# Performance work log

Measured on AMD Instinct MI355X. Metric: run time of the kernel, lower is better.

Reference implementation:

```python
import jax, jax.numpy as jnp
import numpy as np

B, S, IN, OUT, GS = 4, 2048, 4096, 4096, 256
NG = IN // GS  # number of groups per output channel


def setup_inputs() -> dict:
    key = jax.random.key(0)
    k1, k2, k3, k4 = jax.random.split(key, 4)
    x = jax.random.normal(k1, (B, S, IN), dtype=jnp.float32)
    # int4 codes stored in int8: values in [-8, 7]
    weight_int8 = jax.random.randint(k2, (OUT, IN), -8, 8, dtype=jnp.int32).astype(jnp.int8)
    scales = jax.random.uniform(k3, (OUT, NG), dtype=jnp.float32, minval=0.001, maxval=0.02)
    # zero points stored in scales_precision (float), integer-valued in int4 range
    zeros = jax.random.randint(k4, (OUT, NG), -8, 8, dtype=jnp.int32).astype(jnp.float32)
    return {"x": x, "weight_int8": weight_int8, "scales": scales, "zeros": zeros,
            "group_size": GS}


def per_token_dynamic_quant(x):
    """Asymmetric per-token int8 quantize -> dequantize (torchao decomposed ops)."""
    qmin, qmax = -128.0, 127.0
    mn = jnp.minimum(jnp.min(x, axis=-1, keepdims=True), 0.0)
    mx = jnp.maximum(jnp.max(x, axis=-1, keepdims=True), 0.0)
    eps = jnp.finfo(jnp.float32).eps
    scale = jnp.maximum((mx - mn) / (qmax - qmin), eps)
    # choose zero point minimizing error at whichever end is larger
    zp = jnp.where((qmin + mn / scale) + (qmax + mx / scale) > 0,
                   qmin - mn / scale, qmax - mx / scale)
    zp = jnp.clip(jnp.round(zp), qmin, qmax)
    q = jnp.clip(jnp.round(x / scale) + zp, qmin, qmax)
    return (q - zp) * scale


def dequant_per_channel_group(w_int8, scales, zeros, group_size):
    O, I = w_int8.shape
    g = I // group_size
    w = w_int8.reshape(O, g, group_size).astype(jnp.float32)
    w_dq = (w - zeros[:, :, None]) * scales[:, :, None]
    return w_dq.reshape(O, I)


def reference(x, weight_int8, scales, zeros, group_size):
    xq = per_token_dynamic_quant(x.astype(jnp.float32))
    w_dq = dequant_per_channel_group(weight_int8, scales, zeros, group_size)
    # F.linear: x @ w_dq.T  -> [B, S, OUT]
    return jnp.einsum('bsi,oi->bso', xq, w_dq)
```

## Files before the change

kernel.cpp:

```cpp
#include <hip/hip_runtime.h>
#include <hip/hip_bf16.h>
#include <stdint.h>

#define T_   8192
#define IN_  4096
#define OUT_ 4096
#define GS_  256
#define NG_  16

#define BM 128
#define BN 128
#define BK 64
#define KT (IN_ / BK)

typedef int   v4i __attribute__((ext_vector_type(4)));
typedef float f4  __attribute__((ext_vector_type(4)));

__device__ __forceinline__ void gload16(const void* g, void* l) {
  __builtin_amdgcn_global_load_lds(
      (const __attribute__((address_space(1))) void*)g,
      (__attribute__((address_space(3))) void*)l, 16, 0, 0);
}

__global__ __launch_bounds__(256) void quant_kernel(
    const float* __restrict__ x, int8_t* __restrict__ q,
    float* __restrict__ tscale, float* __restrict__ tzp) {
  const int t = blockIdx.x;
  const int tid = threadIdx.x;
  const float* xr = x + (size_t)t * IN_ + tid * 16;
  float vals[16];
  {
    f4 v0 = *(const f4*)(xr);
    f4 v1 = *(const f4*)(xr + 4);
    f4 v2 = *(const f4*)(xr + 8);
    f4 v3 = *(const f4*)(xr + 12);
#pragma unroll
    for (int i = 0; i < 4; ++i) {
      vals[i] = v0[i]; vals[4 + i] = v1[i]; vals[8 + i] = v2[i]; vals[12 + i] = v3[i];
    }
  }
  float mn = 0.f, mx = 0.f;
#pragma unroll
  for (int i = 0; i < 16; ++i) { mn = fminf(mn, vals[i]); mx = fmaxf(mx, vals[i]); }
#pragma unroll
  for (int off = 32; off > 0; off >>= 1) {
    mn = fminf(mn, __shfl_xor(mn, off));
    mx = fmaxf(mx, __shfl_xor(mx, off));
  }
  __shared__ float smn[4], smx[4];
  if ((tid & 63) == 0) { smn[tid >> 6] = mn; smx[tid >> 6] = mx; }
  __syncthreads();
  mn = fminf(fminf(smn[0], smn[1]), fminf(smn[2], smn[3]));
  mx = fmaxf(fmaxf(smx[0], smx[1]), fmaxf(smx[2], smx[3]));

  const float eps = 1.1920928955078125e-7f;
  float scale = fmaxf((mx - mn) / 255.0f, eps);
  float rmn = mn / scale;
  float rmx = mx / scale;
  float zp0 = ((-128.0f + rmn) + (127.0f + rmx) > 0.0f) ? (-128.0f - rmn)
                                                        : (127.0f - rmx);
  float zp = fminf(fmaxf(rintf(zp0), -128.0f), 127.0f);
  if (tid == 0) { tscale[t] = scale; tzp[t] = zp; }

  v4i packed;
#pragma unroll
  for (int w = 0; w < 4; ++w) {
    int word = 0;
#pragma unroll
    for (int e = 0; e < 4; ++e) {
      float qf = rintf(vals[w * 4 + e] / scale) + zp;
      qf = fminf(fmaxf(qf, -128.0f), 127.0f);
      int qi = (int)qf;
      word |= (qi & 0xff) << (8 * e);
    }
    packed[w] = word;
  }
  *(v4i*)(q + (size_t)t * IN_ + tid * 16) = packed;
}

__global__ __launch_bounds__(256) void wprep_kernel(
    const int* __restrict__ w, const float* __restrict__ scales,
    const float* __restrict__ zeros, int8_t* __restrict__ wq,
    float* __restrict__ c1) {
  const int o = blockIdx.x;
  const int tid = threadIdx.x;
  const int g = tid >> 4;
  const int* wr = w + (size_t)o * IN_ + tid * 16;
  const int zi = (int)zeros[o * NG_ + g];
  int ssum = 0;
  v4i packed;
#pragma unroll
  for (int blk = 0; blk < 4; ++blk) {
    v4i ww = *(const v4i*)(wr + blk * 4);
    int word = 0;
#pragma unroll
    for (int e = 0; e < 4; ++e) {
      int wp = ww[e] - zi;
      ssum += wp;
      word |= (wp & 0xff) << (8 * e);
    }
    packed[blk] = word;
  }
  *(v4i*)(wq + (size_t)o * IN_ + tid * 16) = packed;
  ssum += __shfl_xor(ssum, 1);
  ssum += __shfl_xor(ssum, 2);
  ssum += __shfl_xor(ssum, 4);
  ssum += __shfl_xor(ssum, 8);
  __shared__ float part[NG_];
  if ((tid & 15) == 0) part[g] = scales[o * NG_ + g] * (float)ssum;
  __syncthreads();
  if (tid == 0) {
    float s = 0.f;
#pragma unroll
    for (int i = 0; i < NG_; ++i) s += part[i];
    c1[o] = s;
  }
}

__global__ __launch_bounds__(256, 2) void gemm_kernel(
    const int8_t* __restrict__ q, const int8_t* __restrict__ wq,
    const float* __restrict__ scales, const float* __restrict__ tscale,
    const float* __restrict__ tzp, const float* __restrict__ c1,
    float* __restrict__ out) {
  __shared__ int8_t As[BM * BK];
  __shared__ int8_t Bs[BN * BK];
  __shared__ float sSc[NG_ * BN];

  const int tid = threadIdx.x;
  const int lane = tid & 63;
  const int wid = tid >> 6;
  const int R0 = blockIdx.y * BM;
  const int C0 = blockIdx.x * BN;

#pragma unroll
  for (int e = 0; e < 8; ++e) {
    int idx = tid + e * 256;
    int oc = idx >> 4, g = idx & 15;
    sSc[g * BN + oc] = scales[(size_t)(C0 + oc) * NG_ + g];
  }

  const int rowA = tid >> 2;
  const int kb = (tid & 3) * 16;
  const int8_t* gA = q + (size_t)(R0 + rowA) * IN_ + kb;
  const int8_t* gB = wq + (size_t)(C0 + rowA) * IN_ + kb;

  const int wm = (wid >> 1) * 64;
  const int wn = (wid & 1) * 64;
  const int lm = lane & 15;
  const int quad = lane >> 4;

  v4i acci[4][4];
  float accf[4][4][4];
#pragma unroll
  for (int i = 0; i < 4; ++i)
#pragma unroll
    for (int j = 0; j < 4; ++j) {
      acci[i][j] = (v4i){0, 0, 0, 0};
#pragma unroll
      for (int r = 0; r < 4; ++r) accf[i][j][r] = 0.f;
    }

  for (int kt = 0; kt < KT; ++kt) {
    __syncthreads();
    const int koff = kt * BK;
    gload16(gA + koff, &As[tid * 16]);
    gload16(gA + koff + (size_t)64 * IN_, &As[4096 + tid * 16]);
    gload16(gB + koff, &Bs[tid * 16]);
    gload16(gB + koff + (size_t)64 * IN_, &Bs[4096 + tid * 16]);
    __syncthreads();

    v4i af[4], bf[4];
#pragma unroll
    for (int i = 0; i < 4; ++i)
      af[i] = *(const v4i*)&As[(wm + i * 16 + lm) * BK + quad * 16];
#pragma unroll
    for (int j = 0; j < 4; ++j)
      bf[j] = *(const v4i*)&Bs[(wn + j * 16 + lm) * BK + quad * 16];
#pragma unroll
    for (int i = 0; i < 4; ++i)
#pragma unroll
      for (int j = 0; j < 4; ++j)
        acci[i][j] =
            __builtin_amdgcn_mfma_i32_16x16x64_i8(af[i], bf[j], acci[i][j], 0, 0, 0);

    if ((kt & 3) == 3) {
      const int g = kt >> 2;
      float sj[4];
#pragma unroll
      for (int j = 0; j < 4; ++j) sj[j] = sSc[g * BN + wn + j * 16 + lm];
#pragma unroll
      for (int i = 0; i < 4; ++i)
#pragma unroll
        for (int j = 0; j < 4; ++j) {
#pragma unroll
          for (int r = 0; r < 4; ++r)
            accf[i][j][r] += sj[j] * (float)acci[i][j][r];
          acci[i][j] = (v4i){0, 0, 0, 0};
        }
    }
  }

  float cj[4];
#pragma unroll
  for (int j = 0; j < 4; ++j) cj[j] = c1[C0 + wn + j * 16 + lm];
#pragma unroll
  for (int i = 0; i < 4; ++i) {
#pragma unroll
    for (int r = 0; r < 4; ++r) {
      const int row = R0 + wm + i * 16 + quad * 4 + r;
      const float tsc = tscale[row];
      const float tz = tzp[row];
#pragma unroll
      for (int j = 0; j < 4; ++j) {
        const int col = C0 + wn + j * 16 + lm;
        out[(size_t)row * OUT_ + col] = tsc * (accf[i][j][r] - tz * cj[j]);
      }
    }
  }
}

extern "C" void kernel_launch(void* const* d_in, const int* in_sizes, int n_in,
                              void* d_out, int out_size, void* d_ws, size_t ws_size,
                              hipStream_t stream) {
  const float* x = (const float*)d_in[0];
  const int* w = (const int*)d_in[1];
  const float* scales = (const float*)d_in[2];
  const float* zeros = (const float*)d_in[3];

  uint8_t* ws = (uint8_t*)d_ws;
  int8_t* q = (int8_t*)ws;
  int8_t* wq = (int8_t*)(ws + 33554432);
  float* tscale = (float*)(ws + 33554432 + 16777216);
  float* tzp = (float*)(ws + 33554432 + 16777216 + 32768);
  float* c1 = (float*)(ws + 33554432 + 16777216 + 65536);
  float* out = (float*)d_out;

  hipLaunchKernelGGL(quant_kernel, dim3(T_), dim3(256), 0, stream, x, q, tscale, tzp);
  hipLaunchKernelGGL(wprep_kernel, dim3(OUT_), dim3(256), 0, stream, w, scales, zeros, wq, c1);
  hipLaunchKernelGGL(gemm_kernel, dim3(OUT_ / BN, T_ / BM), dim3(256), 0, stream,
                     q, wq, scales, tscale, tzp, c1, out);
}
```

Measured before the change: 445.0 us.

## Double BK to 128 with XOR-swizzled LDS layout and reciprocal quant scale

Doubles the GEMM K-tile to 128, so each barrier pair now covers two MFMA sub-steps and half as many loop iterations run. Global-to-LDS loads use an XOR swizzle of 16-byte chunks by row, and the fragment reads use the matching swizzle, to avoid LDS bank conflicts on the longer rows. The group-scale flush moves to every second tile. The quant kernel also multiplies by a reciprocal instead of dividing, which may change rounding in rare cases.

```diff
diff --git a/kernel.cpp b/kernel.cpp
--- a/kernel.cpp
+++ b/kernel.cpp
@@ -10,7 +10,7 @@
 
 #define BM 128
 #define BN 128
-#define BK 64
+#define BK 128
 #define KT (IN_ / BK)
 
 typedef int   v4i __attribute__((ext_vector_type(4)));
@@ -62,13 +62,14 @@
   float zp = fminf(fmaxf(rintf(zp0), -128.0f), 127.0f);
   if (tid == 0) { tscale[t] = scale; tzp[t] = zp; }
 
+  const float inv = 1.0f / scale;
   v4i packed;
 #pragma unroll
   for (int w = 0; w < 4; ++w) {
     int word = 0;
 #pragma unroll
     for (int e = 0; e < 4; ++e) {
-      float qf = rintf(vals[w * 4 + e] / scale) + zp;
+      float qf = rintf(vals[w * 4 + e] * inv) + zp;
       qf = fminf(fmaxf(qf, -128.0f), 127.0f);
       int qi = (int)qf;
       word |= (qi & 0xff) << (8 * e);
@@ -139,15 +140,18 @@
     sSc[g * BN + oc] = scales[(size_t)(C0 + oc) * NG_ + g];
   }
 
-  const int rowA = tid >> 2;
-  const int kb = (tid & 3) * 16;
-  const int8_t* gA = q + (size_t)(R0 + rowA) * IN_ + kb;
-  const int8_t* gB = wq + (size_t)(C0 + rowA) * IN_ + kb;
+  const int rA = tid >> 3;
+  const int cswz = ((tid & 7) ^ (rA & 7)) * 16;
+  const int8_t* gA = q + (size_t)(R0 + rA) * IN_ + cswz;
+  const int8_t* gB = wq + (size_t)(C0 + rA) * IN_ + cswz;
 
   const int wm = (wid >> 1) * 64;
   const int wn = (wid & 1) * 64;
   const int lm = lane & 15;
   const int quad = lane >> 4;
+  const int o0 = ((quad ^ (lm & 7)) * 16);
+  const int aRow = (wm + lm) * BK;
+  const int bRow = (wn + lm) * BK;
 
   v4i acci[4][4];
   float accf[4][4][4];
@@ -163,28 +167,33 @@
   for (int kt = 0; kt < KT; ++kt) {
     __syncthreads();
     const int koff = kt * BK;
-    gload16(gA + koff, &As[tid * 16]);
-    gload16(gA + koff + (size_t)64 * IN_, &As[4096 + tid * 16]);
-    gload16(gB + koff, &Bs[tid * 16]);
-    gload16(gB + koff + (size_t)64 * IN_, &Bs[4096 + tid * 16]);
+#pragma unroll
+    for (int i = 0; i < 4; ++i) {
+      gload16(gA + koff + (size_t)(i * 32) * IN_, &As[i * 4096 + tid * 16]);
+      gload16(gB + koff + (size_t)(i * 32) * IN_, &Bs[i * 4096 + tid * 16]);
+    }
     __syncthreads();
 
-    v4i af[4], bf[4];
-#pragma unroll
-    for (int i = 0; i < 4; ++i)
-      af[i] = *(const v4i*)&As[(wm + i * 16 + lm) * BK + quad * 16];
-#pragma unroll
-    for (int j = 0; j < 4; ++j)
-      bf[j] = *(const v4i*)&Bs[(wn + j * 16 + lm) * BK + quad * 16];
-#pragma unroll
-    for (int i = 0; i < 4; ++i)
+#pragma unroll
+    for (int ks = 0; ks < 2; ++ks) {
+      const int co = o0 ^ (ks * 64);
+      v4i af[4], bf[4];
+#pragma unroll
+      for (int i = 0; i < 4; ++i)
+        af[i] = *(const v4i*)&As[aRow + i * (16 * BK) + co];
 #pragma unroll
       for (int j = 0; j < 4; ++j)
-        acci[i][j] =
-            __builtin_amdgcn_mfma_i32_16x16x64_i8(af[i], bf[j], acci[i][j], 0, 0, 0);
-
-    if ((kt & 3) == 3) {
-      const int g = kt >> 2;
+        bf[j] = *(const v4i*)&Bs[bRow + j * (16 * BK) + co];
+#pragma unroll
+      for (int i = 0; i < 4; ++i)
+#pragma unroll
+        for (int j = 0; j < 4; ++j)
+          acci[i][j] =
+              __builtin_amdgcn_mfma_i32_16x16x64_i8(af[i], bf[j], acci[i][j], 0, 0, 0);
+    }
+
+    if (kt & 1) {
+      const int g = kt >> 1;
       float sj[4];
 #pragma unroll
       for (int j = 0; j < 4; ++j) sj[j] = sSc[g * BN + wn + j * 16 + lm];
```

New measurement: 430.1 us. 1.03x faster.
